# Optimization experiments

Hardware: AMD Instinct MI355X
Metric: run time of the kernel (lower is better)

The kernel has to match this reference:

```python
import jax, jax.numpy as jnp
from jax import lax
import numpy as np

LOGZERO = -(65504.0 ** 2)  # -torch.finfo(float16).min**2


def setup_inputs() -> dict:
    key = jax.random.key(0)
    ks = jax.random.split(key, 5)
    B, T, D, V, CB, Ly = 32, 512, 512, 4096, 30, 4
    x = jax.random.normal(ks[0], (B, T, D), jnp.float32)
    W = jax.random.normal(ks[1], (V, D), jnp.float32) * 0.02
    b = jax.random.normal(ks[2], (V,), jnp.float32) * 0.02
    xl = jnp.full((B,), T, jnp.int32)
    y = jax.random.randint(ks[3], (B, Ly), 1, V)  # partial hypothesis (last token used)
    # unique candidate ids per row (exclude blank=0) to avoid duplicate-scatter ambiguity
    scores = jax.random.uniform(ks[4], (B, V - 1))
    ctc_beam_idx = jnp.argsort(scores, axis=1)[:, :CB] + 1
    return {"x": x, "W": W, "b": b, "xl": xl, "y": y,
            "ctc_beam_idx": ctc_beam_idx, "blank": 0, "eos": V - 1}


def reference(x, W, b, xl, y, ctc_beam_idx, blank, eos):
    B, T, D = x.shape
    V = W.shape[0]
    CB = ctc_beam_idx.shape[1]
    # forward(): Linear + log_softmax  -> (B, T, V)
    logp = jax.nn.log_softmax(jnp.einsum("btd,vd->btv", x, W) + b, axis=-1)
    # preProcess(): lastP[1] = cumsum of blank logprob over time, lastP[0] = logzero
    blank_lp = logp[:, :, blank]                     # (B, T)
    lastP1 = jnp.cumsum(blank_lp, axis=1).T          # (T, B)
    lastP0 = jnp.full((T, B), LOGZERO, logp.dtype)
    lastPsum = jnp.logaddexp(lastP0, lastP1)         # (T, B)
    # cState.select / bState.select -> candidate and blank scores per beam hyp
    Xn = jnp.take_along_axis(logp, ctc_beam_idx[:, None, :], axis=2)  # (B, T, CB)
    Xn = Xn.transpose(1, 0, 2)                                        # (T, B, CB)
    Xb = jnp.broadcast_to(blank_lp.T[:, :, None], Xn.shape)           # (T, B, CB)
    # prefP: lastPsum everywhere, lastP[1] where candidate == last prediction
    same = (y[:, -1][:, None] == ctc_beam_idx)                        # (B, CB)
    prefP = jnp.where(same[None], lastP1[:, :, None], lastPsum[:, :, None])  # (T, B, CB)
    Ly = y.shape[1]
    start = min(Ly, T - 1)
    loop_start = max(start, 1)
    Pn0 = jnp.full((B, CB), LOGZERO, logp.dtype)
    Pb0 = jnp.full((B, CB), LOGZERO, logp.dtype)
    if start == 0:
        Pn0 = Xn[0]
    def step(carry, inp):
        Pn_prev, Pb_prev = carry
        pref_prev, xn_t, xb_t = inp
        Pn = jnp.logaddexp(Pn_prev, pref_prev) + xn_t
        Pb = jnp.logaddexp(Pn_prev, Pb_prev) + xb_t
        return (Pn, Pb), (Pn, Pb)
    _, (Pn_seq, Pb_seq) = lax.scan(
        step, (Pn0, Pb0),
        (prefP[loop_start - 1:T - 1], Xn[loop_start:], Xb[loop_start:]))
    if start == 0:  # prepend the preset t=0 entry
        Pn_seq = jnp.concatenate([Pn0[None], Pn_seq], axis=0)
        Pb_seq = jnp.concatenate([Pb0[None], Pb_seq], axis=0)
    # curP over t in [start, T)
    curP_t = jnp.logaddexp(Pn_seq, Pb_seq)                            # (T-start, B, CB)
    t_idx = jnp.arange(start, T)
    valid = xl[None, :] > t_idx[:, None]                              # (T-start, B)
    curP_t = jnp.where(valid[:, :, None], curP_t, LOGZERO)
    curP = jax.nn.logsumexp(curP_t, axis=0)                           # (B, CB)
    # scatter into vocab; initial self.prefP == 0.0
    finalP = jnp.full((B, V), LOGZERO, curP.dtype)
    finalP = finalP.at[jnp.arange(B)[:, None], ctc_beam_idx].set(curP)
    # eos score: lastPsum at final valid frame only
    ar = jnp.arange(T)
    maskBT = xl[:, None] > ar[None, :]
    mask0 = (xl - 1)[:, None] > ar[None, :]
    lps = jnp.where(maskBT & ~mask0, lastPsum.T, 0.0)                 # (B, T)
    finalP = finalP.at[:, eos].set(jnp.sum(lps, axis=1))
    finalP = finalP.at[:, blank].set(LOGZERO)
    return finalP
```

## Files before the change

kernel.cpp:

```cpp
#include <hip/hip_runtime.h>
#include <hip/hip_fp8.h>

#define LOGZERO -4290774016.0f
#define L2E 1.4426950408889634f
#define LN2 0.6931471805599453f

constexpr int Bb = 32, Tt = 512, Dd = 512, Vv = 4096;
constexpr int BT = Bb * Tt;

typedef __attribute__((ext_vector_type(4)))  float f32x4;
typedef __attribute__((ext_vector_type(16))) float f32x16;
typedef __attribute__((ext_vector_type(4)))  int   i32x4;
typedef __attribute__((ext_vector_type(8)))  int   i32x8;

#define GLOBAL_AS __attribute__((address_space(1)))
#define LDS_AS    __attribute__((address_space(3)))

__device__ __forceinline__ float fexp2(float x) { return __builtin_amdgcn_exp2f(x); }
__device__ __forceinline__ float flog2(float x) { return __builtin_amdgcn_logf(x); }

__device__ __forceinline__ unsigned cvt4_fp8(float4 v, float s) {
#if __has_builtin(__builtin_amdgcn_cvt_pk_fp8_f32)
  int p = __builtin_amdgcn_cvt_pk_fp8_f32(v.x * s, v.y * s, 0, false);
  p = __builtin_amdgcn_cvt_pk_fp8_f32(v.z * s, v.w * s, p, true);
  return (unsigned)p;
#else
  unsigned b0 = __hip_cvt_float_to_fp8(v.x * s, __HIP_SATFINITE, __HIP_E4M3);
  unsigned b1 = __hip_cvt_float_to_fp8(v.y * s, __HIP_SATFINITE, __HIP_E4M3);
  unsigned b2 = __hip_cvt_float_to_fp8(v.z * s, __HIP_SATFINITE, __HIP_E4M3);
  unsigned b3 = __hip_cvt_float_to_fp8(v.w * s, __HIP_SATFINITE, __HIP_E4M3);
  return b0 | (b1 << 8) | (b2 << 16) | (b3 << 24);
#endif
}

__device__ __forceinline__ float lg2add(float a, float b) {
  float mx = fmaxf(a, b);
  float d  = fabsf(a - b);
  return mx + flog2(1.0f + fexp2(-d));
}

__device__ __forceinline__ i32x8 ld2(const unsigned char* p) {
  i32x4 lo = *(const i32x4*)p;
  i32x4 hx = *(const i32x4*)(p + 1024);
  return __builtin_shufflevector(lo, hx, 0, 1, 2, 3, 4, 5, 6, 7);
}

__global__ __launch_bounds__(256) void kPre(const float* __restrict__ x,
                                            const float* __restrict__ W,
                                            unsigned char* __restrict__ Xfp,
                                            unsigned char* __restrict__ Wp) {
  __shared__ unsigned char T[16384];
  const int tid = threadIdx.x, bid = blockIdx.x;
  const bool isX = bid < 512;
  const float* srcF;
  float scale;
  int cb = 0, half = 0;
  if (isX) {
    srcF = x + (size_t)bid * 32 * Dd;
    scale = 1.0f;
  } else {
    int idx = bid - 512;
    cb = idx >> 1; half = idx & 1;
    srcF = W + ((size_t)cb * 64 + half * 32) * Dd;
    scale = 16.0f;
  }

  #pragma unroll
  for (int p = 0; p < 16; ++p) {
    int f = p * 256 + tid;
    int r = f >> 7;
    int cf = f & 127;
    int c = cf >> 2, m = cf & 3;
    float4 v = *(const float4*)(srcF + (size_t)f * 4);
    unsigned o = cvt4_fp8(v, scale);
    *(unsigned*)(T + ((r * 32 + (c ^ r)) * 16 + m * 4)) = o;
  }
  __syncthreads();

  if (isX) {
    unsigned char* dst = Xfp + (size_t)bid * 16384;
    #pragma unroll
    for (int u = 0; u < 4; ++u) {
      int s = u * 256 + tid;
      int r = s & 31, khalf = (s >> 5) & 1, h = (s >> 6) & 1, kb = s >> 7;
      int c = kb * 4 + khalf * 2 + h;
      uint4 o = *(const uint4*)(T + (r * 32 + (c ^ r)) * 16);
      *(uint4*)(dst + (size_t)s * 16) = o;
    }
  } else {
    unsigned char* dst = Wp + (size_t)cb * 32768;
    #pragma unroll
    for (int u = 0; u < 4; ++u) {
      int lsl = u * 256 + tid;
      int r = lsl & 31, khalf = (lsl >> 5) & 1, h = (lsl >> 6) & 1, kb = lsl >> 7;
      int c = kb * 4 + khalf * 2 + h;
      int s = kb * 256 + half * 128 + h * 64 + khalf * 32 + r;
      uint4 o = *(const uint4*)(T + (r * 32 + (c ^ r)) * 16);
      *(uint4*)(dst + (size_t)s * 16) = o;
    }
  }
}

__global__ __launch_bounds__(256, 4) void kA(const unsigned char* __restrict__ Xfp,
                                             const unsigned char* __restrict__ Wp,
                                             const float* __restrict__ bias,
                                             const int* __restrict__ beam,
                                             const int* __restrict__ blankp,
                                             float* __restrict__ Spart,
                                             float* __restrict__ selL,
                                             int CB) {
  __shared__ unsigned char Ald[32768];
  __shared__ int   selv[31];
  __shared__ float selb[31];

  const int tid = threadIdx.x;
  const int tileN = blockIdx.x & 15;
  const int tileM = blockIdx.x >> 4;
  const int row0 = tileM * 64, col0 = tileN * 256;
  const int bb = row0 >> 9;
  const int lane = tid & 63, w = tid >> 6;
  const int l31 = lane & 31, hi = lane >> 5;

  if (tid < 31) {
    int v = (tid == 0) ? *blankp : beam[bb * CB + tid - 1];
    selv[tid] = v;
    selb[tid] = bias[v];
  }

  const unsigned char* src = Xfp + (size_t)tileM * 32768;
  #pragma unroll
  for (int i = 0; i < 8; ++i) {
    int off = (w * 8 + i) * 1024;
    __builtin_amdgcn_global_load_lds((const GLOBAL_AS void*)(src + off + lane * 16),
                                     (LDS_AS void*)(Ald + off), 16, 0, 0);
  }
  __syncthreads();

  const int colw = col0 + w * 64;
  const int cb = tileN * 4 + w;

  f32x16 acc[2][2];
  #pragma unroll
  for (int ct = 0; ct < 2; ++ct)
    #pragma unroll
    for (int mt = 0; mt < 2; ++mt)
      #pragma unroll
      for (int r = 0; r < 16; ++r) acc[ct][mt][r] = 0.f;

  const unsigned char* wpB = Wp + (size_t)cb * 32768 + lane * 16;
  const unsigned char* aB  = Ald + lane * 16;

  i32x8 bc[2];
  bc[0] = ld2(wpB);
  bc[1] = ld2(wpB + 2048);

  #pragma unroll 1
  for (int kb = 0; kb < 8; ++kb) {
    i32x8 bn[2];
    const int kn = (kb < 7) ? kb + 1 : 7;
    bn[0] = ld2(wpB + kn * 4096);
    bn[1] = ld2(wpB + kn * 4096 + 2048);
    {
      i32x8 af0 = ld2(aB + kb * 2048);
      acc[0][0] = __builtin_amdgcn_mfma_scale_f32_32x32x64_f8f6f4(
          af0, bc[0], acc[0][0], 0, 0, 0, 0x7f7f7f7f, 0, 0x7b7b7b7b);
      acc[1][0] = __builtin_amdgcn_mfma_scale_f32_32x32x64_f8f6f4(
          af0, bc[1], acc[1][0], 0, 0, 0, 0x7f7f7f7f, 0, 0x7b7b7b7b);
    }
    {
      i32x8 af1 = ld2(aB + 16384 + kb * 2048);
      acc[0][1] = __builtin_amdgcn_mfma_scale_f32_32x32x64_f8f6f4(
          af1, bc[0], acc[0][1], 0, 0, 0, 0x7f7f7f7f, 0, 0x7b7b7b7b);
      acc[1][1] = __builtin_amdgcn_mfma_scale_f32_32x32x64_f8f6f4(
          af1, bc[1], acc[1][1], 0, 0, 0, 0x7f7f7f7f, 0, 0x7b7b7b7b);
    }
    bc[0] = bn[0]; bc[1] = bn[1];
  }

  __syncthreads();
  float* P = (float*)Ald;

  float bvl[2];
  #pragma unroll
  for (int ct = 0; ct < 2; ++ct)
    bvl[ct] = bias[colw + ct * 32 + l31] * L2E;

  {
    const int f = w * 32 + l31;
    const int chunk = f >> 2, elem = f & 3;
    #pragma unroll
    for (int mt = 0; mt < 2; ++mt) {
      #pragma unroll
      for (int reg = 0; reg < 16; ++reg) {
        float s = fexp2(acc[0][mt][reg] * L2E + bvl[0]) +
                  fexp2(acc[1][mt][reg] * L2E + bvl[1]);
        int r31 = (reg & 3) + 8 * (reg >> 2) + 4 * hi;
        int row = mt * 32 + r31;
        P[row * 128 + ((chunk ^ r31) << 2) + elem] = s;
      }
    }
  }
  __syncthreads();
  if (tid < 64) {
    const int r31 = tid & 31;
    f32x4 v = {0.f, 0.f, 0.f, 0.f};
    #pragma unroll
    for (int i = 0; i < 32; ++i)
      v += *(const f32x4*)&P[tid * 128 + ((i ^ r31) << 2)];
    Spart[(size_t)tileN * BT + row0 + tid] = v[0] + v[1] + v[2] + v[3];
  }

  const int tbase = row0 & 511;
  #pragma unroll 1
  for (int s = 0; s < 31; ++s) {
    const int vsel = __builtin_amdgcn_readfirstlane(selv[s]);
    const int local = vsel - colw;
    if (local >= 0 && local < 32) {
      const float bvs = selb[s];
      if (l31 == local) {
        #pragma unroll
        for (int mt = 0; mt < 2; ++mt)
          #pragma unroll
          for (int reg = 0; reg < 16; ++reg) {
            int t = tbase + mt * 32 + (reg & 3) + 8 * (reg >> 2) + 4 * hi;
            selL[((size_t)bb * Tt + t) * 31 + s] = acc[0][mt][reg] + bvs;
          }
      }
    } else if (local >= 32 && local < 64) {
      const float bvs = selb[s];
      if (l31 == (local & 31)) {
        #pragma unroll
        for (int mt = 0; mt < 2; ++mt)
          #pragma unroll
          for (int reg = 0; reg < 16; ++reg) {
            int t = tbase + mt * 32 + (reg & 3) + 8 * (reg >> 2) + 4 * hi;
            selL[((size_t)bb * Tt + t) * 31 + s] = acc[1][mt][reg] + bvs;
          }
      }
    }
  }
}

__global__ __launch_bounds__(256) void kC(const float* __restrict__ selL,
                                          const float* __restrict__ Spart,
                                          const int* __restrict__ xl,
                                          const int* __restrict__ beam,
                                          const int* __restrict__ blankp,
                                          const int* __restrict__ eosp,
                                          float* __restrict__ out,
                                          int Ly, int CB) {
  __shared__ float sl[Tt * 31];
  __shared__ float lgS[Tt];
  __shared__ float lastP1[Tt];
  __shared__ float blankLp[Tt];
  const int b = blockIdx.x, tid = threadIdx.x;

  for (int i = tid; i < Tt * 31; i += 256)
    sl[i] = selL[(size_t)b * Tt * 31 + i] * L2E;
  for (int tt = tid; tt < Tt; tt += 256) {
    float s = 0.f;
    #pragma unroll
    for (int n = 0; n < 16; ++n) s += Spart[(size_t)n * BT + b * Tt + tt];
    lgS[tt] = flog2(s);
  }
  __syncthreads();

  float* orow = out + (size_t)b * Vv;
  for (int i = tid; i < Vv; i += 256) orow[i] = LOGZERO;

  const int xlb = xl[b];
  float curP = LOGZERO;
  if (tid < 64) {
    const int lane = tid;
    float vloc[8];
    float run = 0.f;
    #pragma unroll
    for (int u = 0; u < 8; ++u) {
      int t = lane * 8 + u;
      float bl = sl[t * 31] - lgS[t];
      blankLp[t] = bl;
      run += bl;
      vloc[u] = run;
    }
    float inc = run;
    #pragma unroll
    for (int off = 1; off < 64; off <<= 1) {
      float o = __shfl_up(inc, off, 64);
      if (lane >= off) inc += o;
    }
    float excl = inc - run;
    #pragma unroll
    for (int u = 0; u < 8; ++u) lastP1[lane * 8 + u] = vloc[u] + excl;

    const int kk = (lane < CB) ? lane : (CB - 1);
    const float LOG2ZERO = LOGZERO * L2E;
    float Pn = LOG2ZERO, Pb = LOG2ZERO;
    float mrun = -3.0e38f, srun = 0.0f;
    int start = (Ly < Tt - 1) ? Ly : (Tt - 1);
    if (start == 0) {
      Pn = sl[1 + kk] - lgS[0];
      float vv = (0 < xlb) ? lg2add(Pn, Pb) : LOG2ZERO;
      float nm = fmaxf(mrun, vv);
      srun = srun * fexp2(mrun - nm) + fexp2(vv - nm);
      mrun = nm;
    }
    int t0 = (start > 1) ? start : 1;
    float sl_c = sl[t0 * 31 + 1 + kk];
    float lg_c = lgS[t0];
    float xb_c = blankLp[t0];
    float pf_c = lastP1[t0 - 1];
    #pragma unroll 2
    for (int t = t0; t < Tt - 1; ++t) {
      float sl_n = sl[(t + 1) * 31 + 1 + kk];
      float lg_n = lgS[t + 1];
      float xb_n = blankLp[t + 1];
      float pf_n = lastP1[t];
      float xn = sl_c - lg_c;
      float Pn2 = lg2add(Pn, pf_c) + xn;
      float Pb2 = lg2add(Pn, Pb) + xb_c;
      Pn = Pn2; Pb = Pb2;
      float vv = (t < xlb) ? lg2add(Pn, Pb) : LOG2ZERO;
      float nm = fmaxf(mrun, vv);
      srun = srun * fexp2(mrun - nm) + fexp2(vv - nm);
      mrun = nm;
      sl_c = sl_n; lg_c = lg_n; xb_c = xb_n; pf_c = pf_n;
    }
    {
      const int t = Tt - 1;
      float xn = sl_c - lg_c;
      float Pn2 = lg2add(Pn, pf_c) + xn;
      float Pb2 = lg2add(Pn, Pb) + xb_c;
      Pn = Pn2; Pb = Pb2;
      float vv = (t < xlb) ? lg2add(Pn, Pb) : LOG2ZERO;
      float nm = fmaxf(mrun, vv);
      srun = srun * fexp2(mrun - nm) + fexp2(vv - nm);
      mrun = nm;
    }
    curP = (mrun + flog2(srun)) * LN2;
  }
  __syncthreads();

  if (tid < 64) {
    if (tid < CB) orow[beam[b * CB + tid]] = curP;
  }
  __syncthreads();
  if (tid == 0) {
    float eosv = (xlb >= 1) ? lastP1[xlb - 1] * LN2 : 0.0f;
    orow[*eosp] = eosv;
    orow[*blankp] = LOGZERO;
  }
}

extern "C" void kernel_launch(void* const* d_in, const int* in_sizes, int n_in,
                              void* d_out, int out_size, void* d_ws, size_t ws_size,
                              hipStream_t stream) {
  (void)n_in; (void)out_size; (void)ws_size;
  const float* x    = (const float*)d_in[0];
  const float* W    = (const float*)d_in[1];
  const float* bias = (const float*)d_in[2];
  const int* xl     = (const int*)d_in[3];
  const int* beam   = (const int*)d_in[5];
  const int* blankp = (const int*)d_in[6];
  const int* eosp   = (const int*)d_in[7];
  const int Ly = in_sizes[4] / Bb;
  const int CB = in_sizes[5] / Bb;

  float* Spart = (float*)d_ws;
  float* selL  = (float*)((char*)d_ws + (size_t)0x100000);
  unsigned char* Xfp = (unsigned char*)((char*)d_ws + (size_t)0x400000);
  unsigned char* Wp  = (unsigned char*)((char*)d_ws + (size_t)0xC00000);
  float* outf = (float*)d_out;

  kPre<<<640, 256, 0, stream>>>(x, W, Xfp, Wp);
  kA<<<4096, 256, 0, stream>>>(Xfp, Wp, bias, beam, blankp, Spart, selL, CB);
  kC<<<Bb, 256, 0, stream>>>(selL, Spart, xl, beam, blankp, eosp, outf, Ly, CB);
}
```

Baseline: 207.1 us.

## Load A fragments directly from global instead of staging through LDS

Removes the upfront global-to-LDS copy of the 64-row activation tile and the barrier that follows it. Each wave now loads its A fragments straight from global memory in a register double-buffered loop alongside the B fragments. Launch bounds occupancy drops from 4 to 3 blocks to leave room for the extra registers. The four waves in a block each re-read the same A data from global/L2 instead of sharing one LDS copy, and removing the barrier after the MFMA loop assumes the epilogue's reuse of the LDS buffer is still safe.

Result: no change. 209.7 us (+1.2%).

```diff
diff --git a/kernel.cpp b/kernel.cpp
--- a/kernel.cpp
+++ b/kernel.cpp
@@ -101,7 +101,7 @@
   }
 }
 
-__global__ __launch_bounds__(256, 4) void kA(const unsigned char* __restrict__ Xfp,
+__global__ __launch_bounds__(256, 3) void kA(const unsigned char* __restrict__ Xfp,
                                              const unsigned char* __restrict__ Wp,
                                              const float* __restrict__ bias,
                                              const int* __restrict__ beam,
@@ -127,15 +127,6 @@
     selb[tid] = bias[v];
   }
 
-  const unsigned char* src = Xfp + (size_t)tileM * 32768;
-  #pragma unroll
-  for (int i = 0; i < 8; ++i) {
-    int off = (w * 8 + i) * 1024;
-    __builtin_amdgcn_global_load_lds((const GLOBAL_AS void*)(src + off + lane * 16),
-                                     (LDS_AS void*)(Ald + off), 16, 0, 0);
-  }
-  __syncthreads();
-
   const int colw = col0 + w * 64;
   const int cb = tileN * 4 + w;
 
@@ -148,36 +139,31 @@
       for (int r = 0; r < 16; ++r) acc[ct][mt][r] = 0.f;
 
   const unsigned char* wpB = Wp + (size_t)cb * 32768 + lane * 16;
-  const unsigned char* aB  = Ald + lane * 16;
-
-  i32x8 bc[2];
-  bc[0] = ld2(wpB);
-  bc[1] = ld2(wpB + 2048);
+  const unsigned char* aG  = Xfp + (size_t)tileM * 32768 + lane * 16;
+
+  i32x8 bA[2], aA[2];
+  bA[0] = ld2(wpB);       bA[1] = ld2(wpB + 2048);
+  aA[0] = ld2(aG);        aA[1] = ld2(aG + 16384);
 
   #pragma unroll 1
   for (int kb = 0; kb < 8; ++kb) {
-    i32x8 bn[2];
     const int kn = (kb < 7) ? kb + 1 : 7;
-    bn[0] = ld2(wpB + kn * 4096);
-    bn[1] = ld2(wpB + kn * 4096 + 2048);
-    {
-      i32x8 af0 = ld2(aB + kb * 2048);
-      acc[0][0] = __builtin_amdgcn_mfma_scale_f32_32x32x64_f8f6f4(
-          af0, bc[0], acc[0][0], 0, 0, 0, 0x7f7f7f7f, 0, 0x7b7b7b7b);
-      acc[1][0] = __builtin_amdgcn_mfma_scale_f32_32x32x64_f8f6f4(
-          af0, bc[1], acc[1][0], 0, 0, 0, 0x7f7f7f7f, 0, 0x7b7b7b7b);
-    }
-    {
-      i32x8 af1 = ld2(aB + 16384 + kb * 2048);
-      acc[0][1] = __builtin_amdgcn_mfma_scale_f32_32x32x64_f8f6f4(
-          af1, bc[0], acc[0][1], 0, 0, 0, 0x7f7f7f7f, 0, 0x7b7b7b7b);
-      acc[1][1] = __builtin_amdgcn_mfma_scale_f32_32x32x64_f8f6f4(
-          af1, bc[1], acc[1][1], 0, 0, 0, 0x7f7f7f7f, 0, 0x7b7b7b7b);
-    }
-    bc[0] = bn[0]; bc[1] = bn[1];
-  }
-
-  __syncthreads();
+    i32x8 bN[2], aN[2];
+    bN[0] = ld2(wpB + kn * 4096);
+    bN[1] = ld2(wpB + kn * 4096 + 2048);
+    aN[0] = ld2(aG + kn * 2048);
+    aN[1] = ld2(aG + 16384 + kn * 2048);
+    #pragma unroll
+    for (int mt = 0; mt < 2; ++mt) {
+      acc[0][mt] = __builtin_amdgcn_mfma_scale_f32_32x32x64_f8f6f4(
+          aA[mt], bA[0], acc[0][mt], 0, 0, 0, 0x7f7f7f7f, 0, 0x7b7b7b7b);
+      acc[1][mt] = __builtin_amdgcn_mfma_scale_f32_32x32x64_f8f6f4(
+          aA[mt], bA[1], acc[1][mt], 0, 0, 0, 0x7f7f7f7f, 0, 0x7b7b7b7b);
+    }
+    bA[0] = bN[0]; bA[1] = bN[1];
+    aA[0] = aN[0]; aA[1] = aN[1];
+  }
+
   float* P = (float*)Ald;
 
   float bvl[2];
```
